# Performance work log

Hardware: AMD Instinct MI355X
Metric: run time of the kernel (lower is better)

The kernel has to match this reference:

```python
import jax, jax.numpy as jnp
import numpy as np

NH = 8      # num_heads
HD = 16     # head_dim
D = NH * HD # d_model = 128
EPS = 1e-6


def setup_inputs() -> dict:
    key = jax.random.key(0)
    ks = jax.random.split(key, 9)
    B, C, H, W = 8, 128, 128, 128
    t1 = jax.random.normal(ks[0], (B, C, H, W), dtype=jnp.float32)
    t2 = jax.random.normal(ks[1], (B, C, H, W), dtype=jnp.float32)
    t3 = jax.random.normal(ks[2], (B, C, H, W), dtype=jnp.float32)
    fusion_tensor = jax.random.normal(ks[3], (B, C, H, W), dtype=jnp.float32)
    s = 0.05
    Wq = jax.random.normal(ks[4], (D, C), dtype=jnp.float32) * s
    Wk = jax.random.normal(ks[5], (D, C), dtype=jnp.float32) * s
    Wv = jax.random.normal(ks[6], (D, C), dtype=jnp.float32) * s
    Wback = jax.random.normal(ks[7], (C, D), dtype=jnp.float32) * s
    Wout = jax.random.normal(ks[8], (C, 3 * C), dtype=jnp.float32) * s
    return {"t1": t1, "t2": t2, "t3": t3, "fusion_tensor": fusion_tensor,
            "Wq": Wq, "Wk": Wk, "Wv": Wv, "Wback": Wback, "Wout": Wout}


def _to_seq(x):
    # [B,C,H,W] -> [B,N,C]
    B, C, H, W = x.shape
    return x.reshape(B, C, H * W).transpose(0, 2, 1)


def _cross_attn(q_seq, kv_seq, Wq, Wk, Wv, Wback):
    # q_seq, kv_seq: [B,N,C]; 1x1 convs == channel matmuls.
    B, N, _ = q_seq.shape
    q = (q_seq @ Wq.T).reshape(B, N, NH, HD)
    k = (kv_seq @ Wk.T).reshape(B, N, NH, HD)
    v = (kv_seq @ Wv.T).reshape(B, N, NH, HD)
    qh = jax.nn.relu(q) + EPS
    kh = jax.nn.relu(k) + EPS
    kv = jnp.einsum('bnhd,bnhm->bhdm', kh, v)            # [B,NH,HD,HD]
    z = 1.0 / (jnp.einsum('bnhd,bhd->bnh', qh, kh.sum(axis=1)) + EPS)  # [B,N,NH]
    out = jnp.einsum('bnhd,bhdm->bnhm', qh, kv) * z[..., None]
    return out.reshape(B, N, NH * HD) @ Wback.T          # [B,N,C]


def reference(t1, t2, t3, fusion_tensor, Wq, Wk, Wv, Wback, Wout):
    B, C, H, W = t1.shape
    t1s, t2s, t3s = _to_seq(t1), _to_seq(t2), _to_seq(t3)
    fs = _to_seq(fusion_tensor)
    ca = lambda q, kv: _cross_attn(q, kv, Wq, Wk, Wv, Wback)
    # Stage A: pairwise cross-attention among single periods (dropout=0 -> identity)
    t1a = t1s + (ca(t1s, t2s) + ca(t1s, t3s))
    t2a = t2s + (ca(t2s, t1s) + ca(t2s, t3s))
    t3a = t3s + (ca(t3s, t1s) + ca(t3s, t2s))
    # Stage B: each updated period attends to the fusion feature
    t1f = t1a + ca(t1a, fs)
    t2f = t2a + ca(t2a, fs)
    t3f = t3a + ca(t3a, fs)
    concat = jnp.concatenate([t1f, t2f, t3f], axis=-1)   # [B,N,3C]
    fused = concat @ Wout.T + fs                          # [B,N,C]
    return fused.transpose(0, 2, 1).reshape(B, C, H, W)
```

## Files before the change

kernel.cpp:

```cpp
#include <hip/hip_runtime.h>
#include <hip/hip_bf16.h>

#define N_SEQ 16384
#define EPSF 1e-6f

typedef unsigned short u16;
typedef unsigned int   u32;
typedef __attribute__((ext_vector_type(8))) __bf16 bf16x8;
typedef __attribute__((ext_vector_type(4))) float  f32x4;

union B8 { u32 w[4]; bf16x8 v; };

__device__ __forceinline__ int rfl(int x){ return __builtin_amdgcn_readfirstlane(x); }
__device__ __forceinline__ u16 f2b(float x){
  union { __hip_bfloat16 h; u16 u; } c; c.h = __float2bfloat16(x); return c.u;
}
__device__ __forceinline__ u32 pk2(float a, float b){
  return (u32)f2b(a) | ((u32)f2b(b) << 16);
}
__device__ __forceinline__ float bf2f(u16 v){ return __uint_as_float(((u32)v) << 16); }
#define MFMA(a,b,c) __builtin_amdgcn_mfma_f32_16x16x32_bf16((a),(b),(c),0,0,0)

__device__ __forceinline__ int xidx(int n, int f){ return n*128 + (f ^ ((n & 7) << 3)); }
__device__ __forceinline__ int kidx(int d, int n){ return d*64  + (n ^ ((d & 7) << 3)); }

#define QTS 24

__device__ __forceinline__ void gemmW(const u16* __restrict__ Wb, int row, int ldw, int koff,
                                      const u16* __restrict__ Xl, int m, int g, f32x4 q[4]){
  #pragma unroll
  for (int ks = 0; ks < 4; ++ks){
    const bf16x8 av = *reinterpret_cast<const bf16x8*>(&Wb[(size_t)row*ldw + koff + ks*32 + g*8]);
    #pragma unroll
    for (int nt = 0; nt < 4; ++nt){
      const bf16x8 bv = *reinterpret_cast<const bf16x8*>(&Xl[xidx(nt*16+m, ks*32 + g*8)]);
      q[nt] = MFMA(av, bv, q[nt]);
    }
  }
}

template<int NSRC>
__device__ __forceinline__ void stage(u16* Xl, u16* Ul, u16* Qt,
    const u16* __restrict__ wqb, const u16* __restrict__ wbb,
    const u32* __restrict__ kvb, const float* __restrict__ ksf,
    int s1, int s2, int b, int w, int g, int m, int rb){
  const int sA = ((s1*8 + b)*8 + w);
  const int sB = ((s2*8 + b)*8 + w);
  float4 ksA = *reinterpret_cast<const float4*>(ksf + sA*16 + 4*g);
  float4 ksB = ksA;
  B8 kA, kB;
  uint4 ka4 = *reinterpret_cast<const uint4*>(&kvb[sA*128 + (g&1)*64 + m*4]);
  kA.w[0]=ka4.x; kA.w[1]=ka4.y; kA.w[2]=ka4.z; kA.w[3]=ka4.w;
  if (NSRC == 2){
    ksB = *reinterpret_cast<const float4*>(ksf + sB*16 + 4*g);
    uint4 kb4 = *reinterpret_cast<const uint4*>(&kvb[sB*128 + (g&1)*64 + m*4]);
    kB.w[0]=kb4.x; kB.w[1]=kb4.y; kB.w[2]=kb4.z; kB.w[3]=kb4.w;
  }
  f32x4 q[4];
  #pragma unroll
  for (int nt = 0; nt < 4; ++nt) q[nt] = (f32x4){0.f,0.f,0.f,0.f};
  gemmW(wqb, rb + m, 128, 0, Xl, m, g, q);
  #pragma unroll
  for (int nt = 0; nt < 4; ++nt)
    #pragma unroll
    for (int r = 0; r < 4; ++r) q[nt][r] = fmaxf(q[nt][r], 0.f) + EPSF;
  float z1[4], z2[4];
  #pragma unroll
  for (int nt = 0; nt < 4; ++nt){
    float p = q[nt][0]*ksA.x + q[nt][1]*ksA.y + q[nt][2]*ksA.z + q[nt][3]*ksA.w;
    p += __shfl_xor(p, 16); p += __shfl_xor(p, 32);
    z1[nt] = 1.0f / (p + EPSF);
  }
  if (NSRC == 2){
    #pragma unroll
    for (int nt = 0; nt < 4; ++nt){
      float p = q[nt][0]*ksB.x + q[nt][1]*ksB.y + q[nt][2]*ksB.z + q[nt][3]*ksB.w;
      p += __shfl_xor(p, 16); p += __shfl_xor(p, 32);
      z2[nt] = 1.0f / (p + EPSF);
    }
  }
  u16* qrow = Qt + w*(64*QTS);
  #pragma unroll
  for (int nt = 0; nt < 4; ++nt)
    *reinterpret_cast<uint2*>(&qrow[(nt*16+m)*QTS + 4*g]) =
      make_uint2(pk2(q[nt][0], q[nt][1]), pk2(q[nt][2], q[nt][3]));
  #pragma unroll
  for (int nt = 0; nt < 4; ++nt){
    B8 bb;
    if (g < 2) bb.v = *reinterpret_cast<const bf16x8*>(&qrow[(nt*16+m)*QTS + g*8]);
    else { bb.w[0]=0u; bb.w[1]=0u; bb.w[2]=0u; bb.w[3]=0u; }
    const f32x4 z4 = (f32x4){0.f,0.f,0.f,0.f};
    f32x4 S1 = MFMA(kA.v, bb.v, z4);
    f32x4 Uv = S1 * z1[nt];
    if (NSRC == 2){
      f32x4 S2 = MFMA(kB.v, bb.v, z4);
      Uv += S2 * z2[nt];
    }
    *reinterpret_cast<uint2*>(&Ul[xidx(nt*16+m, rb + 4*g)]) =
      make_uint2(pk2(Uv[0], Uv[1]), pk2(Uv[2], Uv[3]));
  }
  f32x4 t4[4];
  #pragma unroll
  for (int nt = 0; nt < 4; ++nt){
    uint2 old = *reinterpret_cast<const uint2*>(&Xl[xidx(nt*16+m, rb + 4*g)]);
    t4[nt][0] = bf2f((u16)(old.x & 0xffffu));
    t4[nt][1] = bf2f((u16)(old.x >> 16));
    t4[nt][2] = bf2f((u16)(old.y & 0xffffu));
    t4[nt][3] = bf2f((u16)(old.y >> 16));
  }
  __syncthreads();
  gemmW(wbb, rb + m, 128, 0, Ul, m, g, t4);
  #pragma unroll
  for (int nt = 0; nt < 4; ++nt)
    *reinterpret_cast<uint2*>(&Xl[xidx(nt*16+m, rb + 4*g)]) =
      make_uint2(pk2(t4[nt][0], t4[nt][1]), pk2(t4[nt][2], t4[nt][3]));
  __syncthreads();
}

__global__ void k_prepack(const float* __restrict__ Wq, const float* __restrict__ Wk,
                          const float* __restrict__ Wv, const float* __restrict__ Wb,
                          const float* __restrict__ Wo,
                          u16* __restrict__ wqb, u16* __restrict__ wkb, u16* __restrict__ wvb,
                          u16* __restrict__ wbb, u16* __restrict__ wob){
  int i = blockIdx.x*256 + threadIdx.x;
  if      (i < 16384) wqb[i]         = f2b(Wq[i]);
  else if (i < 32768) wkb[i - 16384] = f2b(Wk[i - 16384]);
  else if (i < 49152) wvb[i - 32768] = f2b(Wv[i - 32768]);
  else if (i < 65536) wbb[i - 49152] = f2b(Wb[i - 49152]);
  else                wob[i - 65536] = f2b(Wo[i - 65536]);
}

__global__ __launch_bounds__(512, 4) void k_pass1(const float* __restrict__ t1,
    const float* __restrict__ t2, const float* __restrict__ t3, const float* __restrict__ fs,
    const u16* __restrict__ wkb, const u16* __restrict__ wvb,
    float* __restrict__ pkv, float* __restrict__ pks){
  __shared__ u16 Xl [64*128];
  __shared__ u16 khl[128*64];
  __shared__ u16 vl [128*64];
  int bid = blockIdx.x;
  int ch = bid & 15, b = (bid >> 4) & 7, s = bid >> 7;
  int tid = threadIdx.x, lane = tid & 63;
  int w = rfl(tid >> 6), rb = w*16;
  int g = lane >> 4, m = lane & 15;
  const float* src = (s==0)?t1:(s==1)?t2:(s==2)?t3:fs;
  src += (size_t)b*128*N_SEQ + ch*1024;
  f32x4 kvacc = (f32x4){0.f,0.f,0.f,0.f};
  float ksump[4] = {0.f,0.f,0.f,0.f};
  #pragma unroll 1
  for (int tile = 0; tile < 16; ++tile){
    const float* sp = src + tile*64;
    #pragma unroll
    for (int rr = 0; rr < 8; ++rr){
      int c = w*16 + rr*2;
      float f0 = sp[(size_t)c*N_SEQ + lane];
      float f1 = sp[(size_t)(c+1)*N_SEQ + lane];
      *reinterpret_cast<u32*>(&Xl[xidx(lane, c)]) = pk2(f0, f1);
    }
    __syncthreads();
    f32x4 kh[4], vv[4];
    #pragma unroll
    for (int nt = 0; nt < 4; ++nt){ kh[nt] = (f32x4){0.f,0.f,0.f,0.f}; vv[nt] = kh[nt]; }
    gemmW(wkb, rb + m, 128, 0, Xl, m, g, kh);
    gemmW(wvb, rb + m, 128, 0, Xl, m, g, vv);
    #pragma unroll
    for (int nt = 0; nt < 4; ++nt)
      #pragma unroll
      for (int r = 0; r < 4; ++r){
        float x = fmaxf(kh[nt][r], 0.f) + EPSF;
        ksump[r] += x;
        khl[kidx(rb + 4*g + r, nt*16 + m)] = f2b(x);
        vl [kidx(rb + 4*g + r, nt*16 + m)] = f2b(vv[nt][r]);
      }
    __syncthreads();
    #pragma unroll
    for (int ks2 = 0; ks2 < 2; ++ks2){
      const bf16x8 av = *reinterpret_cast<const bf16x8*>(&khl[kidx(rb+m, ks2*32 + g*8)]);
      const bf16x8 bv = *reinterpret_cast<const bf16x8*>(&vl [kidx(rb+m, ks2*32 + g*8)]);
      kvacc = MFMA(av, bv, kvacc);
    }
  }
  size_t pb = (((size_t)(ch*4 + s)*8 + b)*8 + w)*256;
  #pragma unroll
  for (int r = 0; r < 4; ++r)
    pkv[pb + (size_t)(4*g + r)*16 + m] = kvacc[r];
  #pragma unroll
  for (int r = 0; r < 4; ++r){
    float v2 = ksump[r];
    v2 += __shfl_xor(v2, 1); v2 += __shfl_xor(v2, 2);
    v2 += __shfl_xor(v2, 4); v2 += __shfl_xor(v2, 8);
    if (m == 0) pks[(((size_t)(ch*4 + s)*8 + b)*8 + w)*16 + 4*g + r] = v2;
  }
}

__global__ void k_reduce(const float* __restrict__ pkv, const float* __restrict__ pks,
                         u32* __restrict__ kvb, float* __restrict__ ksf){
  int i = blockIdx.x*256 + threadIdx.x;
  if (i < 32768){
    int sA = i >> 7, r7 = i & 127;
    int gb = r7 >> 6, m = (r7 >> 2) & 15, t = r7 & 3;
    int d = gb*8 + 2*t;
    float a0 = 0.f, a1 = 0.f;
    #pragma unroll
    for (int ch = 0; ch < 16; ++ch){
      a0 += pkv[(size_t)ch*65536 + sA*256 + d*16 + m];
      a1 += pkv[(size_t)ch*65536 + sA*256 + (d+1)*16 + m];
    }
    kvb[i] = pk2(a0, a1);
  } else {
    int j = i - 32768;
    float a = 0.f;
    #pragma unroll
    for (int ch = 0; ch < 16; ++ch) a += pks[(size_t)ch*4096 + j];
    ksf[j] = a;
  }
}

__global__ __launch_bounds__(512, 4) void k_pass2(const float* __restrict__ t1,
    const float* __restrict__ t2, const float* __restrict__ t3, const float* __restrict__ fs,
    const u16* __restrict__ wqb, const u16* __restrict__ wbb, const u16* __restrict__ wob,
    const u32* __restrict__ kvb, const float* __restrict__ ksf, float* __restrict__ outp){
  __shared__ u16 Xl[64*128];
  __shared__ u16 Ul[64*128];
  __shared__ u16 Qt[8*64*QTS];
  int bid = blockIdx.x;
  int b = bid >> 8, n0 = (bid & 255) * 64;
  int tid = threadIdx.x, lane = tid & 63;
  int w = rfl(tid >> 6), rb = w*16;
  int g = lane >> 4, m = lane & 15;
  f32x4 oacc[4];
  #pragma unroll
  for (int nt = 0; nt < 4; ++nt) oacc[nt] = (f32x4){0.f,0.f,0.f,0.f};

  #pragma unroll 1
  for (int i = 0; i < 3; ++i){
    const float* src = (i==0)?t1:(i==1)?t2:t3;
    int s1 = (i==0)?1:0, s2 = (i==2)?1:2;
    #pragma unroll
    for (int nt = 0; nt < 4; ++nt){
      float f0 = src[(size_t)(b*128 + rb + 4*g + 0)*N_SEQ + n0 + nt*16 + m];
      float f1 = src[(size_t)(b*128 + rb + 4*g + 1)*N_SEQ + n0 + nt*16 + m];
      float f2 = src[(size_t)(b*128 + rb + 4*g + 2)*N_SEQ + n0 + nt*16 + m];
      float f3 = src[(size_t)(b*128 + rb + 4*g + 3)*N_SEQ + n0 + nt*16 + m];
      *reinterpret_cast<uint2*>(&Xl[xidx(nt*16+m, rb + 4*g)]) =
        make_uint2(pk2(f0, f1), pk2(f2, f3));
    }
    __syncthreads();
    stage<2>(Xl, Ul, Qt, wqb, wbb, kvb, ksf, s1, s2, b, w, g, m, rb);
    stage<1>(Xl, Ul, Qt, wqb, wbb, kvb, ksf, 3, 3, b, w, g, m, rb);
    gemmW(wob, rb + m, 384, i*128, Xl, m, g, oacc);
    __syncthreads();
  }
  #pragma unroll
  for (int nt = 0; nt < 4; ++nt)
    #pragma unroll
    for (int r = 0; r < 4; ++r){
      size_t idx = (size_t)(b*128 + rb + 4*g + r)*N_SEQ + n0 + nt*16 + m;
      outp[idx] = oacc[nt][r] + fs[idx];
    }
}

extern "C" void kernel_launch(void* const* d_in, const int* in_sizes, int n_in,
                              void* d_out, int out_size, void* d_ws, size_t ws_size,
                              hipStream_t stream){
  const float* t1 = (const float*)d_in[0];
  const float* t2 = (const float*)d_in[1];
  const float* t3 = (const float*)d_in[2];
  const float* fs = (const float*)d_in[3];
  const float* Wq = (const float*)d_in[4];
  const float* Wk = (const float*)d_in[5];
  const float* Wv = (const float*)d_in[6];
  const float* Wb = (const float*)d_in[7];
  const float* Wo = (const float*)d_in[8];
  float* outp = (float*)d_out;
  float* ws = (float*)d_ws;
  float* pkv = ws;
  float* pks = ws + 16*65536;
  float* ksf = ws + 16*65536 + 16*4096;
  u32*  kvb  = (u32*)(ksf + 4096);
  u16*  wqb  = (u16*)(kvb + 32768);
  u16*  wkb  = wqb + 16384;
  u16*  wvb  = wkb + 16384;
  u16*  wbb  = wvb + 16384;
  u16*  wob  = wbb + 16384;

  k_prepack<<<dim3(448),  dim3(256), 0, stream>>>(Wq, Wk, Wv, Wb, Wo, wqb, wkb, wvb, wbb, wob);
  k_pass1  <<<dim3(512),  dim3(512), 0, stream>>>(t1, t2, t3, fs, wkb, wvb, pkv, pks);
  k_reduce <<<dim3(144),  dim3(256), 0, stream>>>(pkv, pks, kvb, ksf);
  k_pass2  <<<dim3(2048), dim3(512), 0, stream>>>(t1, t2, t3, fs, wqb, wbb, wob, kvb, ksf, outp);
}
```

Measured before the change: 205.5 us.

## Fold Wback into Wq and Wout to skip residual stream materialization

Precomputes the fused weights Wq·Wback and Wout·Wback in a new prepack kernel. With these, pass2 never has to write the updated residual back to shared memory between stages. Stage-B queries come from qp plus Wq·Wback·U, and the output accumulates Wout-slice·X plus (Wout·Wback)·U for both attention updates. This removes the Wback GEMMs and the intermediate bf16 round-trips of X, at the cost of an extra LDS buffer and a few more GEMMs per iteration. QTS padding also shrinks from 24 to 16.

Measured after the change: 407.9 us. 1.98x slower.

```diff
diff --git a/kernel.cpp b/kernel.cpp
--- a/kernel.cpp
+++ b/kernel.cpp
@@ -24,7 +24,7 @@
 __device__ __forceinline__ int xidx(int n, int f){ return n*128 + (f ^ ((n & 7) << 3)); }
 __device__ __forceinline__ int kidx(int d, int n){ return d*64  + (n ^ ((d & 7) << 3)); }
 
-#define QTS 24
+#define QTS 16
 
 __device__ __forceinline__ void gemmW(const u16* __restrict__ Wb, int row, int ldw, int koff,
                                       const u16* __restrict__ Xl, int m, int g, f32x4 q[4]){
@@ -39,95 +39,29 @@
   }
 }
 
-template<int NSRC>
-__device__ __forceinline__ void stage(u16* Xl, u16* Ul, u16* Qt,
-    const u16* __restrict__ wqb, const u16* __restrict__ wbb,
-    const u32* __restrict__ kvb, const float* __restrict__ ksf,
-    int s1, int s2, int b, int w, int g, int m, int rb){
-  const int sA = ((s1*8 + b)*8 + w);
-  const int sB = ((s2*8 + b)*8 + w);
-  float4 ksA = *reinterpret_cast<const float4*>(ksf + sA*16 + 4*g);
-  float4 ksB = ksA;
-  B8 kA, kB;
-  uint4 ka4 = *reinterpret_cast<const uint4*>(&kvb[sA*128 + (g&1)*64 + m*4]);
-  kA.w[0]=ka4.x; kA.w[1]=ka4.y; kA.w[2]=ka4.z; kA.w[3]=ka4.w;
-  if (NSRC == 2){
-    ksB = *reinterpret_cast<const float4*>(ksf + sB*16 + 4*g);
-    uint4 kb4 = *reinterpret_cast<const uint4*>(&kvb[sB*128 + (g&1)*64 + m*4]);
-    kB.w[0]=kb4.x; kB.w[1]=kb4.y; kB.w[2]=kb4.z; kB.w[3]=kb4.w;
-  }
-  f32x4 q[4];
-  #pragma unroll
-  for (int nt = 0; nt < 4; ++nt) q[nt] = (f32x4){0.f,0.f,0.f,0.f};
-  gemmW(wqb, rb + m, 128, 0, Xl, m, g, q);
-  #pragma unroll
-  for (int nt = 0; nt < 4; ++nt)
-    #pragma unroll
-    for (int r = 0; r < 4; ++r) q[nt][r] = fmaxf(q[nt][r], 0.f) + EPSF;
-  float z1[4], z2[4];
-  #pragma unroll
-  for (int nt = 0; nt < 4; ++nt){
-    float p = q[nt][0]*ksA.x + q[nt][1]*ksA.y + q[nt][2]*ksA.z + q[nt][3]*ksA.w;
-    p += __shfl_xor(p, 16); p += __shfl_xor(p, 32);
-    z1[nt] = 1.0f / (p + EPSF);
-  }
-  if (NSRC == 2){
-    #pragma unroll
-    for (int nt = 0; nt < 4; ++nt){
-      float p = q[nt][0]*ksB.x + q[nt][1]*ksB.y + q[nt][2]*ksB.z + q[nt][3]*ksB.w;
-      p += __shfl_xor(p, 16); p += __shfl_xor(p, 32);
-      z2[nt] = 1.0f / (p + EPSF);
-    }
-  }
-  u16* qrow = Qt + w*(64*QTS);
-  #pragma unroll
-  for (int nt = 0; nt < 4; ++nt)
-    *reinterpret_cast<uint2*>(&qrow[(nt*16+m)*QTS + 4*g]) =
-      make_uint2(pk2(q[nt][0], q[nt][1]), pk2(q[nt][2], q[nt][3]));
-  #pragma unroll
-  for (int nt = 0; nt < 4; ++nt){
-    B8 bb;
-    if (g < 2) bb.v = *reinterpret_cast<const bf16x8*>(&qrow[(nt*16+m)*QTS + g*8]);
-    else { bb.w[0]=0u; bb.w[1]=0u; bb.w[2]=0u; bb.w[3]=0u; }
-    const f32x4 z4 = (f32x4){0.f,0.f,0.f,0.f};
-    f32x4 S1 = MFMA(kA.v, bb.v, z4);
-    f32x4 Uv = S1 * z1[nt];
-    if (NSRC == 2){
-      f32x4 S2 = MFMA(kB.v, bb.v, z4);
-      Uv += S2 * z2[nt];
-    }
-    *reinterpret_cast<uint2*>(&Ul[xidx(nt*16+m, rb + 4*g)]) =
-      make_uint2(pk2(Uv[0], Uv[1]), pk2(Uv[2], Uv[3]));
-  }
-  f32x4 t4[4];
-  #pragma unroll
-  for (int nt = 0; nt < 4; ++nt){
-    uint2 old = *reinterpret_cast<const uint2*>(&Xl[xidx(nt*16+m, rb + 4*g)]);
-    t4[nt][0] = bf2f((u16)(old.x & 0xffffu));
-    t4[nt][1] = bf2f((u16)(old.x >> 16));
-    t4[nt][2] = bf2f((u16)(old.y & 0xffffu));
-    t4[nt][3] = bf2f((u16)(old.y >> 16));
-  }
-  __syncthreads();
-  gemmW(wbb, rb + m, 128, 0, Ul, m, g, t4);
-  #pragma unroll
-  for (int nt = 0; nt < 4; ++nt)
-    *reinterpret_cast<uint2*>(&Xl[xidx(nt*16+m, rb + 4*g)]) =
-      make_uint2(pk2(t4[nt][0], t4[nt][1]), pk2(t4[nt][2], t4[nt][3]));
-  __syncthreads();
-}
-
 __global__ void k_prepack(const float* __restrict__ Wq, const float* __restrict__ Wk,
-                          const float* __restrict__ Wv, const float* __restrict__ Wb,
-                          const float* __restrict__ Wo,
+                          const float* __restrict__ Wv, const float* __restrict__ Wo,
                           u16* __restrict__ wqb, u16* __restrict__ wkb, u16* __restrict__ wvb,
-                          u16* __restrict__ wbb, u16* __restrict__ wob){
+                          u16* __restrict__ wob){
   int i = blockIdx.x*256 + threadIdx.x;
   if      (i < 16384) wqb[i]         = f2b(Wq[i]);
   else if (i < 32768) wkb[i - 16384] = f2b(Wk[i - 16384]);
   else if (i < 49152) wvb[i - 32768] = f2b(Wv[i - 32768]);
-  else if (i < 65536) wbb[i - 49152] = f2b(Wb[i - 49152]);
-  else                wob[i - 65536] = f2b(Wo[i - 65536]);
+  else                wob[i - 49152] = f2b(Wo[i - 49152]);
+}
+
+__global__ void k_prepack2(const float* __restrict__ Wq, const float* __restrict__ Wb,
+                           const float* __restrict__ Wo,
+                           u16* __restrict__ wqwb, u16* __restrict__ wowb){
+  int i = blockIdx.x*256 + threadIdx.x;
+  int mtx = i >> 14;
+  int r = (i >> 7) & 127, c = i & 127;
+  const float* A = (mtx == 0) ? (Wq + (size_t)r*128) : (Wo + (size_t)r*384 + (mtx-1)*128);
+  float acc = 0.f;
+  #pragma unroll 4
+  for (int k = 0; k < 128; ++k) acc += A[k] * Wb[k*128 + c];
+  if (mtx == 0) wqwb[r*128 + c] = f2b(acc);
+  else          wowb[(size_t)(mtx-1)*16384 + r*128 + c] = f2b(acc);
 }
 
 __global__ __launch_bounds__(512, 4) void k_pass1(const float* __restrict__ t1,
@@ -217,16 +151,26 @@
 
 __global__ __launch_bounds__(512, 4) void k_pass2(const float* __restrict__ t1,
     const float* __restrict__ t2, const float* __restrict__ t3, const float* __restrict__ fs,
-    const u16* __restrict__ wqb, const u16* __restrict__ wbb, const u16* __restrict__ wob,
+    const u16* __restrict__ wqb, const u16* __restrict__ wob,
+    const u16* __restrict__ wqwb, const u16* __restrict__ wowb,
     const u32* __restrict__ kvb, const float* __restrict__ ksf, float* __restrict__ outp){
   __shared__ u16 Xl[64*128];
-  __shared__ u16 Ul[64*128];
+  __shared__ u16 Ua[64*128];
+  __shared__ u16 Ub[64*128];
   __shared__ u16 Qt[8*64*QTS];
   int bid = blockIdx.x;
   int b = bid >> 8, n0 = (bid & 255) * 64;
   int tid = threadIdx.x, lane = tid & 63;
   int w = rfl(tid >> 6), rb = w*16;
   int g = lane >> 4, m = lane & 15;
+  u16* qrow = Qt + w*(64*QTS);
+
+  const int sF = ((3*8 + b)*8 + w);
+  float4 ksF = *reinterpret_cast<const float4*>(ksf + sF*16 + 4*g);
+  B8 kF;
+  { uint4 k4 = *reinterpret_cast<const uint4*>(&kvb[sF*128 + (g&1)*64 + m*4]);
+    kF.w[0]=k4.x; kF.w[1]=k4.y; kF.w[2]=k4.z; kF.w[3]=k4.w; }
+
   f32x4 oacc[4];
   #pragma unroll
   for (int nt = 0; nt < 4; ++nt) oacc[nt] = (f32x4){0.f,0.f,0.f,0.f};
@@ -235,6 +179,8 @@
   for (int i = 0; i < 3; ++i){
     const float* src = (i==0)?t1:(i==1)?t2:t3;
     int s1 = (i==0)?1:0, s2 = (i==2)?1:2;
+    const int sA = ((s1*8 + b)*8 + w);
+    const int sB = ((s2*8 + b)*8 + w);
     #pragma unroll
     for (int nt = 0; nt < 4; ++nt){
       float f0 = src[(size_t)(b*128 + rb + 4*g + 0)*N_SEQ + n0 + nt*16 + m];
@@ -245,10 +191,75 @@
         make_uint2(pk2(f0, f1), pk2(f2, f3));
     }
     __syncthreads();
-    stage<2>(Xl, Ul, Qt, wqb, wbb, kvb, ksf, s1, s2, b, w, g, m, rb);
-    stage<1>(Xl, Ul, Qt, wqb, wbb, kvb, ksf, 3, 3, b, w, g, m, rb);
+    f32x4 qp[4];
+    #pragma unroll
+    for (int nt = 0; nt < 4; ++nt) qp[nt] = (f32x4){0.f,0.f,0.f,0.f};
+    gemmW(wqb, rb + m, 128, 0, Xl, m, g, qp);
     gemmW(wob, rb + m, 384, i*128, Xl, m, g, oacc);
-    __syncthreads();
+    {
+      float4 ksA = *reinterpret_cast<const float4*>(ksf + sA*16 + 4*g);
+      float4 ksB = *reinterpret_cast<const float4*>(ksf + sB*16 + 4*g);
+      B8 kA, kB;
+      uint4 a4 = *reinterpret_cast<const uint4*>(&kvb[sA*128 + (g&1)*64 + m*4]);
+      kA.w[0]=a4.x; kA.w[1]=a4.y; kA.w[2]=a4.z; kA.w[3]=a4.w;
+      uint4 b4 = *reinterpret_cast<const uint4*>(&kvb[sB*128 + (g&1)*64 + m*4]);
+      kB.w[0]=b4.x; kB.w[1]=b4.y; kB.w[2]=b4.z; kB.w[3]=b4.w;
+      f32x4 q[4];
+      float z1[4], z2[4];
+      #pragma unroll
+      for (int nt = 0; nt < 4; ++nt){
+        #pragma unroll
+        for (int r = 0; r < 4; ++r) q[nt][r] = fmaxf(qp[nt][r], 0.f) + EPSF;
+        float p1 = q[nt][0]*ksA.x + q[nt][1]*ksA.y + q[nt][2]*ksA.z + q[nt][3]*ksA.w;
+        p1 += __shfl_xor(p1, 16); p1 += __shfl_xor(p1, 32);
+        z1[nt] = 1.0f / (p1 + EPSF);
+        float p2 = q[nt][0]*ksB.x + q[nt][1]*ksB.y + q[nt][2]*ksB.z + q[nt][3]*ksB.w;
+        p2 += __shfl_xor(p2, 16); p2 += __shfl_xor(p2, 32);
+        z2[nt] = 1.0f / (p2 + EPSF);
+        *reinterpret_cast<uint2*>(&qrow[(nt*16+m)*QTS + 4*g]) =
+          make_uint2(pk2(q[nt][0], q[nt][1]), pk2(q[nt][2], q[nt][3]));
+      }
+      #pragma unroll
+      for (int nt = 0; nt < 4; ++nt){
+        B8 bb;
+        if (g < 2) bb.v = *reinterpret_cast<const bf16x8*>(&qrow[(nt*16+m)*QTS + g*8]);
+        else { bb.w[0]=0u; bb.w[1]=0u; bb.w[2]=0u; bb.w[3]=0u; }
+        const f32x4 z4 = (f32x4){0.f,0.f,0.f,0.f};
+        f32x4 Uv = MFMA(kA.v, bb.v, z4) * z1[nt];
+        Uv += MFMA(kB.v, bb.v, z4) * z2[nt];
+        *reinterpret_cast<uint2*>(&Ua[xidx(nt*16+m, rb + 4*g)]) =
+          make_uint2(pk2(Uv[0], Uv[1]), pk2(Uv[2], Uv[3]));
+      }
+    }
+    __syncthreads();
+    gemmW(wqwb, rb + m, 128, 0, Ua, m, g, qp);
+    gemmW(wowb + (size_t)i*16384, rb + m, 128, 0, Ua, m, g, oacc);
+    {
+      f32x4 q[4];
+      float zf[4];
+      #pragma unroll
+      for (int nt = 0; nt < 4; ++nt){
+        #pragma unroll
+        for (int r = 0; r < 4; ++r) q[nt][r] = fmaxf(qp[nt][r], 0.f) + EPSF;
+        float p = q[nt][0]*ksF.x + q[nt][1]*ksF.y + q[nt][2]*ksF.z + q[nt][3]*ksF.w;
+        p += __shfl_xor(p, 16); p += __shfl_xor(p, 32);
+        zf[nt] = 1.0f / (p + EPSF);
+        *reinterpret_cast<uint2*>(&qrow[(nt*16+m)*QTS + 4*g]) =
+          make_uint2(pk2(q[nt][0], q[nt][1]), pk2(q[nt][2], q[nt][3]));
+      }
+      #pragma unroll
+      for (int nt = 0; nt < 4; ++nt){
+        B8 bb;
+        if (g < 2) bb.v = *reinterpret_cast<const bf16x8*>(&qrow[(nt*16+m)*QTS + g*8]);
+        else { bb.w[0]=0u; bb.w[1]=0u; bb.w[2]=0u; bb.w[3]=0u; }
+        const f32x4 z4 = (f32x4){0.f,0.f,0.f,0.f};
+        f32x4 Uv = MFMA(kF.v, bb.v, z4) * zf[nt];
+        *reinterpret_cast<uint2*>(&Ub[xidx(nt*16+m, rb + 4*g)]) =
+          make_uint2(pk2(Uv[0], Uv[1]), pk2(Uv[2], Uv[3]));
+      }
+    }
+    __syncthreads();
+    gemmW(wowb + (size_t)i*16384, rb + m, 128, 0, Ub, m, g, oacc);
   }
   #pragma unroll
   for (int nt = 0; nt < 4; ++nt)
@@ -275,16 +286,19 @@
   float* ws = (float*)d_ws;
   float* pkv = ws;
   float* pks = ws + 16*65536;
-  float* ksf = ws + 16*65536 + 16*4096;
+  float* ksf = pks + 16*4096;
   u32*  kvb  = (u32*)(ksf + 4096);
   u16*  wqb  = (u16*)(kvb + 32768);
   u16*  wkb  = wqb + 16384;
   u16*  wvb  = wkb + 16384;
-  u16*  wbb  = wvb + 16384;
-  u16*  wob  = wbb + 16384;
-
-  k_prepack<<<dim3(448),  dim3(256), 0, stream>>>(Wq, Wk, Wv, Wb, Wo, wqb, wkb, wvb, wbb, wob);
-  k_pass1  <<<dim3(512),  dim3(512), 0, stream>>>(t1, t2, t3, fs, wkb, wvb, pkv, pks);
-  k_reduce <<<dim3(144),  dim3(256), 0, stream>>>(pkv, pks, kvb, ksf);
-  k_pass2  <<<dim3(2048), dim3(512), 0, stream>>>(t1, t2, t3, fs, wqb, wbb, wob, kvb, ksf, outp);
-}
+  u16*  wob  = wvb + 16384;
+  u16*  wqwb = wob + 49152;
+  u16*  wowb = wqwb + 16384;
+
+  k_prepack <<<dim3(384),  dim3(256), 0, stream>>>(Wq, Wk, Wv, Wo, wqb, wkb, wvb, wob);
+  k_prepack2<<<dim3(256),  dim3(256), 0, stream>>>(Wq, Wb, Wo, wqwb, wowb);
+  k_pass1   <<<dim3(512),  dim3(512), 0, stream>>>(t1, t2, t3, fs, wkb, wvb, pkv, pks);
+  k_reduce  <<<dim3(144),  dim3(256), 0, stream>>>(pkv, pks, kvb, ksf);
+  k_pass2   <<<dim3(2048), dim3(512), 0, stream>>>(t1, t2, t3, fs, wqb, wob, wqwb, wowb,
+                                                   kvb, ksf, outp);
+}
```

## Halve pass2 block to 4 waves, each computing two heads per wave

Applied to the files above, without the earlier changes.

k_pass2 now launches 256 threads instead of 512, and each wave handles 32 output rows (two heads) rather than 16. A new gemmW2 helper reuses each LDS B-fragment load across two MFMAs, one per weight-row tile. This cuts LDS traffic per MFMA and halves barrier participants, at the cost of more accumulator registers (launch bounds changed to 256,3) and fewer waves available to hide latency. The Qt row stride shrinks from 24 to 16, which may add LDS bank conflicts.

Measured after the change: 387.6 us. 88.6% more time.

```diff
diff --git a/kernel.cpp b/kernel.cpp
--- a/kernel.cpp
+++ b/kernel.cpp
@@ -24,7 +24,7 @@
 __device__ __forceinline__ int xidx(int n, int f){ return n*128 + (f ^ ((n & 7) << 3)); }
 __device__ __forceinline__ int kidx(int d, int n){ return d*64  + (n ^ ((d & 7) << 3)); }
 
-#define QTS 24
+#define QTS 16
 
 __device__ __forceinline__ void gemmW(const u16* __restrict__ Wb, int row, int ldw, int koff,
                                       const u16* __restrict__ Xl, int m, int g, f32x4 q[4]){
@@ -35,6 +35,22 @@
     for (int nt = 0; nt < 4; ++nt){
       const bf16x8 bv = *reinterpret_cast<const bf16x8*>(&Xl[xidx(nt*16+m, ks*32 + g*8)]);
       q[nt] = MFMA(av, bv, q[nt]);
+    }
+  }
+}
+
+__device__ __forceinline__ void gemmW2(const u16* __restrict__ Wb, int row0, int ldw, int koff,
+                                       const u16* __restrict__ Xl, int m, int g,
+                                       f32x4 q0[4], f32x4 q1[4]){
+  #pragma unroll
+  for (int ks = 0; ks < 4; ++ks){
+    const bf16x8 av0 = *reinterpret_cast<const bf16x8*>(&Wb[(size_t)row0*ldw + koff + ks*32 + g*8]);
+    const bf16x8 av1 = *reinterpret_cast<const bf16x8*>(&Wb[(size_t)(row0+16)*ldw + koff + ks*32 + g*8]);
+    #pragma unroll
+    for (int nt = 0; nt < 4; ++nt){
+      const bf16x8 bv = *reinterpret_cast<const bf16x8*>(&Xl[xidx(nt*16+m, ks*32 + g*8)]);
+      q0[nt] = MFMA(av0, bv, q0[nt]);
+      q1[nt] = MFMA(av1, bv, q1[nt]);
     }
   }
 }
@@ -44,76 +60,78 @@
     const u16* __restrict__ wqb, const u16* __restrict__ wbb,
     const u32* __restrict__ kvb, const float* __restrict__ ksf,
     int s1, int s2, int b, int w, int g, int m, int rb){
-  const int sA = ((s1*8 + b)*8 + w);
-  const int sB = ((s2*8 + b)*8 + w);
-  float4 ksA = *reinterpret_cast<const float4*>(ksf + sA*16 + 4*g);
-  float4 ksB = ksA;
-  B8 kA, kB;
-  uint4 ka4 = *reinterpret_cast<const uint4*>(&kvb[sA*128 + (g&1)*64 + m*4]);
-  kA.w[0]=ka4.x; kA.w[1]=ka4.y; kA.w[2]=ka4.z; kA.w[3]=ka4.w;
-  if (NSRC == 2){
-    ksB = *reinterpret_cast<const float4*>(ksf + sB*16 + 4*g);
-    uint4 kb4 = *reinterpret_cast<const uint4*>(&kvb[sB*128 + (g&1)*64 + m*4]);
-    kB.w[0]=kb4.x; kB.w[1]=kb4.y; kB.w[2]=kb4.z; kB.w[3]=kb4.w;
-  }
-  f32x4 q[4];
-  #pragma unroll
-  for (int nt = 0; nt < 4; ++nt) q[nt] = (f32x4){0.f,0.f,0.f,0.f};
-  gemmW(wqb, rb + m, 128, 0, Xl, m, g, q);
-  #pragma unroll
-  for (int nt = 0; nt < 4; ++nt)
-    #pragma unroll
-    for (int r = 0; r < 4; ++r) q[nt][r] = fmaxf(q[nt][r], 0.f) + EPSF;
-  float z1[4], z2[4];
+  f32x4 q0[4], q1[4];
+  #pragma unroll
+  for (int nt = 0; nt < 4; ++nt){ q0[nt] = (f32x4){0.f,0.f,0.f,0.f}; q1[nt] = q0[nt]; }
+  gemmW2(wqb, rb + m, 128, 0, Xl, m, g, q0, q1);
+  #pragma unroll
+  for (int j = 0; j < 2; ++j){
+    const int h = 2*w + j;
+    const int rbh = rb + 16*j;
+    u16* qrow = Qt + h*(64*QTS);
+    const int sA = ((s1*8 + b)*8 + h);
+    float4 ksA = *reinterpret_cast<const float4*>(ksf + sA*16 + 4*g);
+    B8 kA, kB;
+    uint4 a4 = *reinterpret_cast<const uint4*>(&kvb[sA*128 + (g&1)*64 + m*4]);
+    kA.w[0]=a4.x; kA.w[1]=a4.y; kA.w[2]=a4.z; kA.w[3]=a4.w;
+    float4 ksB = ksA;
+    if (NSRC == 2){
+      const int sB = ((s2*8 + b)*8 + h);
+      ksB = *reinterpret_cast<const float4*>(ksf + sB*16 + 4*g);
+      uint4 b4 = *reinterpret_cast<const uint4*>(&kvb[sB*128 + (g&1)*64 + m*4]);
+      kB.w[0]=b4.x; kB.w[1]=b4.y; kB.w[2]=b4.z; kB.w[3]=b4.w;
+    }
+    #pragma unroll
+    for (int nt = 0; nt < 4; ++nt){
+      f32x4 qv = j ? q1[nt] : q0[nt];
+      float a0 = fmaxf(qv[0], 0.f) + EPSF;
+      float a1 = fmaxf(qv[1], 0.f) + EPSF;
+      float a2 = fmaxf(qv[2], 0.f) + EPSF;
+      float a3 = fmaxf(qv[3], 0.f) + EPSF;
+      float p1 = a0*ksA.x + a1*ksA.y + a2*ksA.z + a3*ksA.w;
+      p1 += __shfl_xor(p1, 16); p1 += __shfl_xor(p1, 32);
+      float z1 = 1.0f / (p1 + EPSF);
+      float z2 = 0.f;
+      if (NSRC == 2){
+        float p2 = a0*ksB.x + a1*ksB.y + a2*ksB.z + a3*ksB.w;
+        p2 += __shfl_xor(p2, 16); p2 += __shfl_xor(p2, 32);
+        z2 = 1.0f / (p2 + EPSF);
+      }
+      *reinterpret_cast<uint2*>(&qrow[(nt*16+m)*QTS + 4*g]) =
+        make_uint2(pk2(a0, a1), pk2(a2, a3));
+      B8 bb;
+      if (g < 2) bb.v = *reinterpret_cast<const bf16x8*>(&qrow[(nt*16+m)*QTS + g*8]);
+      else { bb.w[0]=0u; bb.w[1]=0u; bb.w[2]=0u; bb.w[3]=0u; }
+      const f32x4 z4 = (f32x4){0.f,0.f,0.f,0.f};
+      f32x4 Uv = MFMA(kA.v, bb.v, z4) * z1;
+      if (NSRC == 2) Uv += MFMA(kB.v, bb.v, z4) * z2;
+      *reinterpret_cast<uint2*>(&Ul[xidx(nt*16+m, rbh + 4*g)]) =
+        make_uint2(pk2(Uv[0], Uv[1]), pk2(Uv[2], Uv[3]));
+    }
+  }
+  f32x4 t40[4], t41[4];
   #pragma unroll
   for (int nt = 0; nt < 4; ++nt){
-    float p = q[nt][0]*ksA.x + q[nt][1]*ksA.y + q[nt][2]*ksA.z + q[nt][3]*ksA.w;
-    p += __shfl_xor(p, 16); p += __shfl_xor(p, 32);
-    z1[nt] = 1.0f / (p + EPSF);
-  }
-  if (NSRC == 2){
-    #pragma unroll
-    for (int nt = 0; nt < 4; ++nt){
-      float p = q[nt][0]*ksB.x + q[nt][1]*ksB.y + q[nt][2]*ksB.z + q[nt][3]*ksB.w;
-      p += __shfl_xor(p, 16); p += __shfl_xor(p, 32);
-      z2[nt] = 1.0f / (p + EPSF);
-    }
-  }
-  u16* qrow = Qt + w*(64*QTS);
-  #pragma unroll
-  for (int nt = 0; nt < 4; ++nt)
-    *reinterpret_cast<uint2*>(&qrow[(nt*16+m)*QTS + 4*g]) =
-      make_uint2(pk2(q[nt][0], q[nt][1]), pk2(q[nt][2], q[nt][3]));
+    uint2 o0 = *reinterpret_cast<const uint2*>(&Xl[xidx(nt*16+m, rb + 4*g)]);
+    uint2 o1 = *reinterpret_cast<const uint2*>(&Xl[xidx(nt*16+m, rb + 16 + 4*g)]);
+    t40[nt][0] = bf2f((u16)(o0.x & 0xffffu));
+    t40[nt][1] = bf2f((u16)(o0.x >> 16));
+    t40[nt][2] = bf2f((u16)(o0.y & 0xffffu));
+    t40[nt][3] = bf2f((u16)(o0.y >> 16));
+    t41[nt][0] = bf2f((u16)(o1.x & 0xffffu));
+    t41[nt][1] = bf2f((u16)(o1.x >> 16));
+    t41[nt][2] = bf2f((u16)(o1.y & 0xffffu));
+    t41[nt][3] = bf2f((u16)(o1.y >> 16));
+  }
+  __syncthreads();
+  gemmW2(wbb, rb + m, 128, 0, Ul, m, g, t40, t41);
   #pragma unroll
   for (int nt = 0; nt < 4; ++nt){
-    B8 bb;
-    if (g < 2) bb.v = *reinterpret_cast<const bf16x8*>(&qrow[(nt*16+m)*QTS + g*8]);
-    else { bb.w[0]=0u; bb.w[1]=0u; bb.w[2]=0u; bb.w[3]=0u; }
-    const f32x4 z4 = (f32x4){0.f,0.f,0.f,0.f};
-    f32x4 S1 = MFMA(kA.v, bb.v, z4);
-    f32x4 Uv = S1 * z1[nt];
-    if (NSRC == 2){
-      f32x4 S2 = MFMA(kB.v, bb.v, z4);
-      Uv += S2 * z2[nt];
-    }
-    *reinterpret_cast<uint2*>(&Ul[xidx(nt*16+m, rb + 4*g)]) =
-      make_uint2(pk2(Uv[0], Uv[1]), pk2(Uv[2], Uv[3]));
-  }
-  f32x4 t4[4];
-  #pragma unroll
-  for (int nt = 0; nt < 4; ++nt){
-    uint2 old = *reinterpret_cast<const uint2*>(&Xl[xidx(nt*16+m, rb + 4*g)]);
-    t4[nt][0] = bf2f((u16)(old.x & 0xffffu));
-    t4[nt][1] = bf2f((u16)(old.x >> 16));
-    t4[nt][2] = bf2f((u16)(old.y & 0xffffu));
-    t4[nt][3] = bf2f((u16)(old.y >> 16));
-  }
-  __syncthreads();
-  gemmW(wbb, rb + m, 128, 0, Ul, m, g, t4);
-  #pragma unroll
-  for (int nt = 0; nt < 4; ++nt)
     *reinterpret_cast<uint2*>(&Xl[xidx(nt*16+m, rb + 4*g)]) =
-      make_uint2(pk2(t4[nt][0], t4[nt][1]), pk2(t4[nt][2], t4[nt][3]));
+      make_uint2(pk2(t40[nt][0], t40[nt][1]), pk2(t40[nt][2], t40[nt][3]));
+    *reinterpret_cast<uint2*>(&Xl[xidx(nt*16+m, rb + 16 + 4*g)]) =
+      make_uint2(pk2(t41[nt][0], t41[nt][1]), pk2(t41[nt][2], t41[nt][3]));
+  }
   __syncthreads();
 }
 
@@ -215,7 +233,7 @@
   }
 }
 
-__global__ __launch_bounds__(512, 4) void k_pass2(const float* __restrict__ t1,
+__global__ __launch_bounds__(256, 3) void k_pass2(const float* __restrict__ t1,
     const float* __restrict__ t2, const float* __restrict__ t3, const float* __restrict__ fs,
     const u16* __restrict__ wqb, const u16* __restrict__ wbb, const u16* __restrict__ wob,
     const u32* __restrict__ kvb, const float* __restrict__ ksf, float* __restrict__ outp){
@@ -225,37 +243,43 @@
   int bid = blockIdx.x;
   int b = bid >> 8, n0 = (bid & 255) * 64;
   int tid = threadIdx.x, lane = tid & 63;
-  int w = rfl(tid >> 6), rb = w*16;
+  int w = rfl(tid >> 6), rb = w*32;
   int g = lane >> 4, m = lane & 15;
-  f32x4 oacc[4];
-  #pragma unroll
-  for (int nt = 0; nt < 4; ++nt) oacc[nt] = (f32x4){0.f,0.f,0.f,0.f};
+  f32x4 oac0[4], oac1[4];
+  #pragma unroll
+  for (int nt = 0; nt < 4; ++nt){ oac0[nt] = (f32x4){0.f,0.f,0.f,0.f}; oac1[nt] = oac0[nt]; }
 
   #pragma unroll 1
   for (int i = 0; i < 3; ++i){
     const float* src = (i==0)?t1:(i==1)?t2:t3;
     int s1 = (i==0)?1:0, s2 = (i==2)?1:2;
     #pragma unroll
-    for (int nt = 0; nt < 4; ++nt){
-      float f0 = src[(size_t)(b*128 + rb + 4*g + 0)*N_SEQ + n0 + nt*16 + m];
-      float f1 = src[(size_t)(b*128 + rb + 4*g + 1)*N_SEQ + n0 + nt*16 + m];
-      float f2 = src[(size_t)(b*128 + rb + 4*g + 2)*N_SEQ + n0 + nt*16 + m];
-      float f3 = src[(size_t)(b*128 + rb + 4*g + 3)*N_SEQ + n0 + nt*16 + m];
-      *reinterpret_cast<uint2*>(&Xl[xidx(nt*16+m, rb + 4*g)]) =
-        make_uint2(pk2(f0, f1), pk2(f2, f3));
+    for (int half = 0; half < 2; ++half){
+      int rbh = rb + 16*half;
+      #pragma unroll
+      for (int nt = 0; nt < 4; ++nt){
+        float f0 = src[(size_t)(b*128 + rbh + 4*g + 0)*N_SEQ + n0 + nt*16 + m];
+        float f1 = src[(size_t)(b*128 + rbh + 4*g + 1)*N_SEQ + n0 + nt*16 + m];
+        float f2 = src[(size_t)(b*128 + rbh + 4*g + 2)*N_SEQ + n0 + nt*16 + m];
+        float f3 = src[(size_t)(b*128 + rbh + 4*g + 3)*N_SEQ + n0 + nt*16 + m];
+        *reinterpret_cast<uint2*>(&Xl[xidx(nt*16+m, rbh + 4*g)]) =
+          make_uint2(pk2(f0, f1), pk2(f2, f3));
+      }
     }
     __syncthreads();
     stage<2>(Xl, Ul, Qt, wqb, wbb, kvb, ksf, s1, s2, b, w, g, m, rb);
     stage<1>(Xl, Ul, Qt, wqb, wbb, kvb, ksf, 3, 3, b, w, g, m, rb);
-    gemmW(wob, rb + m, 384, i*128, Xl, m, g, oacc);
+    gemmW2(wob, rb + m, 384, i*128, Xl, m, g, oac0, oac1);
     __syncthreads();
   }
   #pragma unroll
   for (int nt = 0; nt < 4; ++nt)
     #pragma unroll
     for (int r = 0; r < 4; ++r){
-      size_t idx = (size_t)(b*128 + rb + 4*g + r)*N_SEQ + n0 + nt*16 + m;
-      outp[idx] = oacc[nt][r] + fs[idx];
+      size_t i0 = (size_t)(b*128 + rb + 4*g + r)*N_SEQ + n0 + nt*16 + m;
+      size_t i1 = (size_t)(b*128 + rb + 16 + 4*g + r)*N_SEQ + n0 + nt*16 + m;
+      outp[i0] = oac0[nt][r] + fs[i0];
+      outp[i1] = oac1[nt][r] + fs[i1];
     }
 }
 
@@ -286,5 +310,5 @@
   k_prepack<<<dim3(448),  dim3(256), 0, stream>>>(Wq, Wk, Wv, Wb, Wo, wqb, wkb, wvb, wbb, wob);
   k_pass1  <<<dim3(512),  dim3(512), 0, stream>>>(t1, t2, t3, fs, wkb, wvb, pkv, pks);
   k_reduce <<<dim3(144),  dim3(256), 0, stream>>>(pkv, pks, kvb, ksf);
-  k_pass2  <<<dim3(2048), dim3(512), 0, stream>>>(t1, t2, t3, fs, wqb, wbb, wob, kvb, ksf, outp);
-}
+  k_pass2  <<<dim3(2048), dim3(256), 0, stream>>>(t1, t2, t3, fs, wqb, wbb, wob, kvb, ksf, outp);
+}
```

## Switch pass2 GEMMs to 32x32x16 MFMA with 2D wave tiling

Applied to the files above, without the earlier changes.

Pass 2 now splits the 64x128 block tile across waves as 32x32 sub-tiles (two heads per wave, half the rows) and uses the 32x32x16 bf16 MFMA for the Q, back-projection and output GEMMs. Each wave loads half as many weight rows per output element and issues fewer, larger MFMAs, which is meant to cut LDS and global weight traffic per flop. The per-head normalisation now needs cross-lane shuffles to redistribute z, and the Qt padding is reduced to 16, which may bring LDS bank conflicts back. Register pressure from the 16-wide accumulators could also limit occupancy.

Measured after the change: 583.9 us. 2.84x slower.

```diff
diff --git a/kernel.cpp b/kernel.cpp
--- a/kernel.cpp
+++ b/kernel.cpp
@@ -6,8 +6,9 @@
 
 typedef unsigned short u16;
 typedef unsigned int   u32;
-typedef __attribute__((ext_vector_type(8))) __bf16 bf16x8;
-typedef __attribute__((ext_vector_type(4))) float  f32x4;
+typedef __attribute__((ext_vector_type(8)))  __bf16 bf16x8;
+typedef __attribute__((ext_vector_type(4)))  float  f32x4;
+typedef __attribute__((ext_vector_type(16))) float  f32x16;
 
 union B8 { u32 w[4]; bf16x8 v; };
 
@@ -19,12 +20,13 @@
   return (u32)f2b(a) | ((u32)f2b(b) << 16);
 }
 __device__ __forceinline__ float bf2f(u16 v){ return __uint_as_float(((u32)v) << 16); }
-#define MFMA(a,b,c) __builtin_amdgcn_mfma_f32_16x16x32_bf16((a),(b),(c),0,0,0)
+#define MFMA(a,b,c)   __builtin_amdgcn_mfma_f32_16x16x32_bf16((a),(b),(c),0,0,0)
+#define MFMA32(a,b,c) __builtin_amdgcn_mfma_f32_32x32x16_bf16((a),(b),(c),0,0,0)
 
 __device__ __forceinline__ int xidx(int n, int f){ return n*128 + (f ^ ((n & 7) << 3)); }
 __device__ __forceinline__ int kidx(int d, int n){ return d*64  + (n ^ ((d & 7) << 3)); }
 
-#define QTS 24
+#define QTS 16
 
 __device__ __forceinline__ void gemmW(const u16* __restrict__ Wb, int row, int ldw, int koff,
                                       const u16* __restrict__ Xl, int m, int g, f32x4 q[4]){
@@ -39,81 +41,93 @@
   }
 }
 
+__device__ __forceinline__ void gemm32(const u16* __restrict__ Wb, int rb32, int ldw, int koff,
+                                       const u16* __restrict__ Xl, int CB, int lm, int l5,
+                                       f32x16& acc){
+  #pragma unroll
+  for (int ks = 0; ks < 8; ++ks){
+    const bf16x8 av = *reinterpret_cast<const bf16x8*>(
+        &Wb[(size_t)(rb32 + lm)*ldw + koff + ks*16 + l5*8]);
+    const bf16x8 bv = *reinterpret_cast<const bf16x8*>(
+        &Xl[xidx(CB + lm, ks*16 + l5*8)]);
+    acc = MFMA32(av, bv, acc);
+  }
+}
+
 template<int NSRC>
-__device__ __forceinline__ void stage(u16* Xl, u16* Ul, u16* Qt,
+__device__ __forceinline__ void stage32(u16* Xl, u16* Ul, u16* Qt,
     const u16* __restrict__ wqb, const u16* __restrict__ wbb,
     const u32* __restrict__ kvb, const float* __restrict__ ksf,
-    int s1, int s2, int b, int w, int g, int m, int rb){
-  const int sA = ((s1*8 + b)*8 + w);
-  const int sB = ((s2*8 + b)*8 + w);
-  float4 ksA = *reinterpret_cast<const float4*>(ksf + sA*16 + 4*g);
-  float4 ksB = ksA;
-  B8 kA, kB;
-  uint4 ka4 = *reinterpret_cast<const uint4*>(&kvb[sA*128 + (g&1)*64 + m*4]);
-  kA.w[0]=ka4.x; kA.w[1]=ka4.y; kA.w[2]=ka4.z; kA.w[3]=ka4.w;
-  if (NSRC == 2){
-    ksB = *reinterpret_cast<const float4*>(ksf + sB*16 + 4*g);
-    uint4 kb4 = *reinterpret_cast<const uint4*>(&kvb[sB*128 + (g&1)*64 + m*4]);
-    kB.w[0]=kb4.x; kB.w[1]=kb4.y; kB.w[2]=kb4.z; kB.w[3]=kb4.w;
-  }
-  f32x4 q[4];
-  #pragma unroll
-  for (int nt = 0; nt < 4; ++nt) q[nt] = (f32x4){0.f,0.f,0.f,0.f};
-  gemmW(wqb, rb + m, 128, 0, Xl, m, g, q);
-  #pragma unroll
-  for (int nt = 0; nt < 4; ++nt)
-    #pragma unroll
-    for (int r = 0; r < 4; ++r) q[nt][r] = fmaxf(q[nt][r], 0.f) + EPSF;
-  float z1[4], z2[4];
-  #pragma unroll
-  for (int nt = 0; nt < 4; ++nt){
-    float p = q[nt][0]*ksA.x + q[nt][1]*ksA.y + q[nt][2]*ksA.z + q[nt][3]*ksA.w;
-    p += __shfl_xor(p, 16); p += __shfl_xor(p, 32);
-    z1[nt] = 1.0f / (p + EPSF);
-  }
-  if (NSRC == 2){
-    #pragma unroll
-    for (int nt = 0; nt < 4; ++nt){
-      float p = q[nt][0]*ksB.x + q[nt][1]*ksB.y + q[nt][2]*ksB.z + q[nt][3]*ksB.w;
-      p += __shfl_xor(p, 16); p += __shfl_xor(p, 32);
-      z2[nt] = 1.0f / (p + EPSF);
-    }
-  }
-  u16* qrow = Qt + w*(64*QTS);
-  #pragma unroll
-  for (int nt = 0; nt < 4; ++nt)
-    *reinterpret_cast<uint2*>(&qrow[(nt*16+m)*QTS + 4*g]) =
-      make_uint2(pk2(q[nt][0], q[nt][1]), pk2(q[nt][2], q[nt][3]));
-  #pragma unroll
-  for (int nt = 0; nt < 4; ++nt){
-    B8 bb;
-    if (g < 2) bb.v = *reinterpret_cast<const bf16x8*>(&qrow[(nt*16+m)*QTS + g*8]);
-    else { bb.w[0]=0u; bb.w[1]=0u; bb.w[2]=0u; bb.w[3]=0u; }
-    const f32x4 z4 = (f32x4){0.f,0.f,0.f,0.f};
-    f32x4 S1 = MFMA(kA.v, bb.v, z4);
-    f32x4 Uv = S1 * z1[nt];
+    int s1, int s2, int b, int W, int CB, int lm, int l5, int g, int m, int rb32){
+  f32x16 q;
+  #pragma unroll
+  for (int r = 0; r < 16; ++r) q[r] = 0.f;
+  gemm32(wqb, rb32, 128, 0, Xl, CB, lm, l5, q);
+  #pragma unroll
+  for (int r = 0; r < 16; ++r) q[r] = fmaxf(q[r], 0.f) + EPSF;
+  #pragma unroll
+  for (int j = 0; j < 2; ++j){
+    const int h  = 2*W + j;
+    const int qb = 8*j;
+    const int sA = ((s1*8 + b)*8 + h);
+    const int sB = ((s2*8 + b)*8 + h);
+    float4 a0 = *reinterpret_cast<const float4*>(ksf + sA*16 + 4*l5);
+    float4 a1 = *reinterpret_cast<const float4*>(ksf + sA*16 + 8 + 4*l5);
+    float p1 = q[qb+0]*a0.x + q[qb+1]*a0.y + q[qb+2]*a0.z + q[qb+3]*a0.w
+             + q[qb+4]*a1.x + q[qb+5]*a1.y + q[qb+6]*a1.z + q[qb+7]*a1.w;
+    p1 += __shfl_xor(p1, 32);
+    float z1 = 1.0f / (p1 + EPSF);
+    float z2 = 0.f;
     if (NSRC == 2){
-      f32x4 S2 = MFMA(kB.v, bb.v, z4);
-      Uv += S2 * z2[nt];
-    }
-    *reinterpret_cast<uint2*>(&Ul[xidx(nt*16+m, rb + 4*g)]) =
-      make_uint2(pk2(Uv[0], Uv[1]), pk2(Uv[2], Uv[3]));
-  }
-  f32x4 t4[4];
-  #pragma unroll
-  for (int nt = 0; nt < 4; ++nt){
-    uint2 old = *reinterpret_cast<const uint2*>(&Xl[xidx(nt*16+m, rb + 4*g)]);
-    t4[nt][0] = bf2f((u16)(old.x & 0xffffu));
-    t4[nt][1] = bf2f((u16)(old.x >> 16));
-    t4[nt][2] = bf2f((u16)(old.y & 0xffffu));
-    t4[nt][3] = bf2f((u16)(old.y >> 16));
+      float4 b0 = *reinterpret_cast<const float4*>(ksf + sB*16 + 4*l5);
+      float4 b1 = *reinterpret_cast<const float4*>(ksf + sB*16 + 8 + 4*l5);
+      float p2 = q[qb+0]*b0.x + q[qb+1]*b0.y + q[qb+2]*b0.z + q[qb+3]*b0.w
+               + q[qb+4]*b1.x + q[qb+5]*b1.y + q[qb+6]*b1.z + q[qb+7]*b1.w;
+      p2 += __shfl_xor(p2, 32);
+      z2 = 1.0f / (p2 + EPSF);
+    }
+    u16* qrow = Qt + h*(64*QTS) + (CB + lm)*QTS;
+    *reinterpret_cast<uint2*>(&qrow[4*l5]) =
+      make_uint2(pk2(q[qb+0], q[qb+1]), pk2(q[qb+2], q[qb+3]));
+    *reinterpret_cast<uint2*>(&qrow[8 + 4*l5]) =
+      make_uint2(pk2(q[qb+4], q[qb+5]), pk2(q[qb+6], q[qb+7]));
+    B8 kA, kB;
+    uint4 ka4 = *reinterpret_cast<const uint4*>(&kvb[sA*128 + (g&1)*64 + m*4]);
+    kA.w[0]=ka4.x; kA.w[1]=ka4.y; kA.w[2]=ka4.z; kA.w[3]=ka4.w;
+    if (NSRC == 2){
+      uint4 kb4 = *reinterpret_cast<const uint4*>(&kvb[sB*128 + (g&1)*64 + m*4]);
+      kB.w[0]=kb4.x; kB.w[1]=kb4.y; kB.w[2]=kb4.z; kB.w[3]=kb4.w;
+    }
+    #pragma unroll
+    for (int nt = 0; nt < 2; ++nt){
+      float zp1 = __shfl(z1, nt*16 + m);
+      float zp2 = (NSRC == 2) ? __shfl(z2, nt*16 + m) : 0.f;
+      B8 bb;
+      if (g < 2) bb.v = *reinterpret_cast<const bf16x8*>(
+          &Qt[h*(64*QTS) + (CB + nt*16 + m)*QTS + g*8]);
+      else { bb.w[0]=0u; bb.w[1]=0u; bb.w[2]=0u; bb.w[3]=0u; }
+      const f32x4 z4 = (f32x4){0.f,0.f,0.f,0.f};
+      f32x4 Uv = MFMA(kA.v, bb.v, z4) * zp1;
+      if (NSRC == 2) Uv += MFMA(kB.v, bb.v, z4) * zp2;
+      *reinterpret_cast<uint2*>(&Ul[xidx(CB + nt*16 + m, h*16 + 4*g)]) =
+        make_uint2(pk2(Uv[0], Uv[1]), pk2(Uv[2], Uv[3]));
+    }
+  }
+  f32x16 t4;
+  #pragma unroll
+  for (int rg = 0; rg < 4; ++rg){
+    uint2 o = *reinterpret_cast<const uint2*>(&Xl[xidx(CB + lm, rb32 + 8*rg + 4*l5)]);
+    t4[4*rg+0] = bf2f((u16)(o.x & 0xffffu));
+    t4[4*rg+1] = bf2f((u16)(o.x >> 16));
+    t4[4*rg+2] = bf2f((u16)(o.y & 0xffffu));
+    t4[4*rg+3] = bf2f((u16)(o.y >> 16));
   }
   __syncthreads();
-  gemmW(wbb, rb + m, 128, 0, Ul, m, g, t4);
-  #pragma unroll
-  for (int nt = 0; nt < 4; ++nt)
-    *reinterpret_cast<uint2*>(&Xl[xidx(nt*16+m, rb + 4*g)]) =
-      make_uint2(pk2(t4[nt][0], t4[nt][1]), pk2(t4[nt][2], t4[nt][3]));
+  gemm32(wbb, rb32, 128, 0, Ul, CB, lm, l5, t4);
+  #pragma unroll
+  for (int rg = 0; rg < 4; ++rg)
+    *reinterpret_cast<uint2*>(&Xl[xidx(CB + lm, rb32 + 8*rg + 4*l5)]) =
+      make_uint2(pk2(t4[4*rg+0], t4[4*rg+1]), pk2(t4[4*rg+2], t4[4*rg+3]));
   __syncthreads();
 }
 
@@ -225,37 +239,41 @@
   int bid = blockIdx.x;
   int b = bid >> 8, n0 = (bid & 255) * 64;
   int tid = threadIdx.x, lane = tid & 63;
-  int w = rfl(tid >> 6), rb = w*16;
+  int w = rfl(tid >> 6);
+  int W = w >> 1, CB = (w & 1) * 32, rb32 = W * 32;
+  int lm = lane & 31, l5 = lane >> 5;
   int g = lane >> 4, m = lane & 15;
-  f32x4 oacc[4];
-  #pragma unroll
-  for (int nt = 0; nt < 4; ++nt) oacc[nt] = (f32x4){0.f,0.f,0.f,0.f};
+  f32x16 oacc;
+  #pragma unroll
+  for (int r = 0; r < 16; ++r) oacc[r] = 0.f;
 
   #pragma unroll 1
   for (int i = 0; i < 3; ++i){
     const float* src = (i==0)?t1:(i==1)?t2:t3;
     int s1 = (i==0)?1:0, s2 = (i==2)?1:2;
     #pragma unroll
-    for (int nt = 0; nt < 4; ++nt){
-      float f0 = src[(size_t)(b*128 + rb + 4*g + 0)*N_SEQ + n0 + nt*16 + m];
-      float f1 = src[(size_t)(b*128 + rb + 4*g + 1)*N_SEQ + n0 + nt*16 + m];
-      float f2 = src[(size_t)(b*128 + rb + 4*g + 2)*N_SEQ + n0 + nt*16 + m];
-      float f3 = src[(size_t)(b*128 + rb + 4*g + 3)*N_SEQ + n0 + nt*16 + m];
-      *reinterpret_cast<uint2*>(&Xl[xidx(nt*16+m, rb + 4*g)]) =
-        make_uint2(pk2(f0, f1), pk2(f2, f3));
+    for (int rg = 0; rg < 4; ++rg){
+      int f = rb32 + 8*rg + 4*l5;
+      float v0 = src[(size_t)(b*128 + f + 0)*N_SEQ + n0 + CB + lm];
+      float v1 = src[(size_t)(b*128 + f + 1)*N_SEQ + n0 + CB + lm];
+      float v2 = src[(size_t)(b*128 + f + 2)*N_SEQ + n0 + CB + lm];
+      float v3 = src[(size_t)(b*128 + f + 3)*N_SEQ + n0 + CB + lm];
+      *reinterpret_cast<uint2*>(&Xl[xidx(CB + lm, f)]) =
+        make_uint2(pk2(v0, v1), pk2(v2, v3));
     }
     __syncthreads();
-    stage<2>(Xl, Ul, Qt, wqb, wbb, kvb, ksf, s1, s2, b, w, g, m, rb);
-    stage<1>(Xl, Ul, Qt, wqb, wbb, kvb, ksf, 3, 3, b, w, g, m, rb);
-    gemmW(wob, rb + m, 384, i*128, Xl, m, g, oacc);
+    stage32<2>(Xl, Ul, Qt, wqb, wbb, kvb, ksf, s1, s2, b, W, CB, lm, l5, g, m, rb32);
+    stage32<1>(Xl, Ul, Qt, wqb, wbb, kvb, ksf, 3, 3, b, W, CB, lm, l5, g, m, rb32);
+    gemm32(wob, rb32, 384, i*128, Xl, CB, lm, l5, oacc);
     __syncthreads();
   }
   #pragma unroll
-  for (int nt = 0; nt < 4; ++nt)
-    #pragma unroll
-    for (int r = 0; r < 4; ++r){
-      size_t idx = (size_t)(b*128 + rb + 4*g + r)*N_SEQ + n0 + nt*16 + m;
-      outp[idx] = oacc[nt][r] + fs[idx];
+  for (int rg = 0; rg < 4; ++rg)
+    #pragma unroll
+    for (int rr = 0; rr < 4; ++rr){
+      int f = rb32 + 8*rg + 4*l5 + rr;
+      size_t idx = (size_t)(b*128 + f)*N_SEQ + n0 + CB + lm;
+      outp[idx] = oacc[4*rg + rr] + fs[idx];
     }
 }
 
```
